# Performance work log

Measured on AMD Instinct MI355X. Metric: run time of the kernel, lower is better.

## Reference

```python
import jax, jax.numpy as jnp
import numpy as np
from jax import lax

DIM = 256
STATE = 64
D_INNER = 256          # ssd_expand=1 * dim
HIDDEN = 4 * DIM       # mlp_ratio=4
CONV_DIM = 3 * STATE
B, H, W = 16, 64, 64
EPS = 1e-5


def dwconv(x, w, b=None):
    # depthwise 3x3, SAME padding; x:(B,C,H,W) w:(C,1,3,3)
    y = lax.conv_general_dilated(x, w, (1, 1), 'SAME',
                                 feature_group_count=x.shape[1],
                                 dimension_numbers=('NCHW', 'OIHW', 'NCHW'))
    if b is not None:
        y = y + b[None, :, None, None]
    return y


def batchnorm(x, g, b):
    m = x.mean(axis=(0, 2, 3), keepdims=True)
    v = x.var(axis=(0, 2, 3), keepdims=True)
    return (x - m) * jax.lax.rsqrt(v + EPS) * g[None, :, None, None] + b[None, :, None, None]


def layernorm1d(x, w, b):
    # norm over channel dim of (B,C,L)
    m = x.mean(axis=1, keepdims=True)
    v = x.var(axis=1, keepdims=True)
    return (x - m) * jax.lax.rsqrt(v + EPS) * w[None, :, None] + b[None, :, None]


def pw1d(x, w, b):
    # 1x1 conv1d: x:(B,Cin,L), w:(Cout,Cin)
    return jnp.einsum('oc,bcl->bol', w, x) + b[None, :, None]


def setup_inputs() -> dict:
    key = jax.random.key(0)
    ks = jax.random.split(key, 16)
    s = 0.02
    inp = {
        'x': jax.random.normal(ks[0], (B, DIM, H, W), jnp.float32),
        'alpha': 1e-4 * jnp.ones((4, DIM), jnp.float32),
        'dw1_w': s * jax.random.normal(ks[1], (DIM, 1, 3, 3), jnp.float32),
        'bn1_g': jnp.ones((DIM,), jnp.float32),
        'bn1_b': jnp.zeros((DIM,), jnp.float32),
        'dw2_w': s * jax.random.normal(ks[2], (DIM, 1, 3, 3), jnp.float32),
        'bn2_g': jnp.ones((DIM,), jnp.float32),
        'bn2_b': jnp.zeros((DIM,), jnp.float32),
        'ln_w': jnp.ones((DIM,), jnp.float32),
        'ln_b': jnp.zeros((DIM,), jnp.float32),
        'bcdt_w': s * jax.random.normal(ks[3], (CONV_DIM, DIM), jnp.float32),
        'bcdt_b': jnp.zeros((CONV_DIM,), jnp.float32),
        'mdw_w': s * jax.random.normal(ks[4], (CONV_DIM, 1, 3, 3), jnp.float32),
        'mdw_b': jnp.zeros((CONV_DIM,), jnp.float32),
        'hz_w': s * jax.random.normal(ks[5], (2 * D_INNER, DIM), jnp.float32),
        'hz_b': jnp.zeros((2 * D_INNER,), jnp.float32),
        'out_w': s * jax.random.normal(ks[6], (DIM, D_INNER), jnp.float32),
        'out_b': jnp.zeros((DIM,), jnp.float32),
        'A': jax.random.uniform(ks[7], (STATE,), jnp.float32, 1.0, 16.0),
        'D': jnp.ones((1,), jnp.float32),
        'ffn_w1': s * jax.random.normal(ks[8], (HIDDEN, DIM), jnp.float32),
        'ffn_b1': jnp.zeros((HIDDEN,), jnp.float32),
        'ffn_w2': s * jax.random.normal(ks[9], (DIM, HIDDEN), jnp.float32),
        'ffn_b2': jnp.zeros((DIM,), jnp.float32),
    }
    return inp


def _mixer(xf, bcdt_w, bcdt_b, mdw_w, mdw_b, hz_w, hz_b, out_w, out_b, A, D, h_, w_):
    # xf: (B, dim, L)
    b = xf.shape[0]
    BCdt = pw1d(xf, bcdt_w, bcdt_b).reshape(b, CONV_DIM, h_, w_)
    BCdt = dwconv(BCdt, mdw_w, mdw_b).reshape(b, CONV_DIM, h_ * w_)
    Bm, Cm, dt = jnp.split(BCdt, [STATE, 2 * STATE], axis=1)  # (B,S,L) each
    Am = jax.nn.softmax(dt + A[None, :, None], axis=-1)
    AB = Am * Bm                                   # (B,S,L)
    h = jnp.einsum('bcl,bsl->bcs', xf, AB)         # (B,dim,S) small
    hz = jnp.einsum('oc,bcs->bos', hz_w, h) + hz_b[None, :, None]
    hh, z = jnp.split(hz, [D_INNER], axis=1)
    hh = hh * jax.nn.silu(z) + hh * D[0]
    hh = jnp.einsum('oc,bcs->bos', out_w, hh) + out_b[None, :, None]
    y = jnp.einsum('bcs,bsl->bcl', hh, Cm)         # (B,dim,L)
    return y.reshape(b, DIM, h_, w_)


def reference(x, alpha, dw1_w, bn1_g, bn1_b, dw2_w, bn2_g, bn2_b, ln_w, ln_b,
              bcdt_w, bcdt_b, mdw_w, mdw_b, hz_w, hz_b, out_w, out_b, A, D,
              ffn_w1, ffn_b1, ffn_w2, ffn_b2):
    a = jax.nn.sigmoid(alpha)[:, None, :, None, None]  # (4,1,dim,1,1)
    x = (1 - a[0]) * x + a[0] * batchnorm(dwconv(x, dw1_w), bn1_g, bn1_b)
    x_prev = x
    b, _, h_, w_ = x.shape
    xf = layernorm1d(x.reshape(b, DIM, h_ * w_), ln_w, ln_b)
    y = _mixer(xf, bcdt_w, bcdt_b, mdw_w, mdw_b, hz_w, hz_b, out_w, out_b, A, D, h_, w_)
    x = (1 - a[1]) * x_prev + a[1] * y
    x = (1 - a[2]) * x + a[2] * batchnorm(dwconv(x, dw2_w), bn2_g, bn2_b)
    # FFN: 1x1 conv -> GELU -> 1x1 conv
    hdn = jax.nn.gelu(jnp.einsum('oc,bchw->bohw', ffn_w1, x) + ffn_b1[None, :, None, None])
    x_ffn = jnp.einsum('oc,bchw->bohw', ffn_w2, hdn) + ffn_b2[None, :, None, None]
    x = (1 - a[3]) * x + a[3] * x_ffn
    return x
```

## Files before the change

### kernel.cpp

```cpp
#include <hip/hip_runtime.h>
#include <stdint.h>


typedef __attribute__((ext_vector_type(8))) short bf16x8;
typedef __attribute__((ext_vector_type(4))) float f32x4;

__device__ __forceinline__ unsigned short f2b(float f){
  union { float f; unsigned int u; } v; v.f = f;
  unsigned int r = v.u + 0x7FFFu + ((v.u >> 16) & 1u);
  return (unsigned short)(r >> 16);
}
__device__ __forceinline__ float b2f(unsigned short h){
  union { unsigned int u; float f; } v; v.u = ((unsigned int)h) << 16;
  return v.f;
}
__device__ __forceinline__ float sigm(float x){ return 1.0f / (1.0f + __expf(-x)); }
__device__ __forceinline__ float gelu_fast(float v){
  float t = v * (-2.3022059f - 0.10294886f * v * v);
  float e = __builtin_amdgcn_exp2f(t);
  return v * __builtin_amdgcn_rcpf(1.0f + e);
}
__device__ __forceinline__ unsigned int cvtpk(float lo, float hi){
  unsigned int r;
  asm volatile("v_cvt_pk_bf16_f32 %0, %1, %2" : "=v"(r) : "v"(lo), "v"(hi));
  return r;
}
__device__ __forceinline__ f32x4 mfma16(bf16x8 a, bf16x8 b, f32x4 c){
  return __builtin_amdgcn_mfma_f32_16x16x32_bf16(a, b, c, 0, 0, 0);
}
__device__ __forceinline__ bf16x8 ldb8g(const unsigned short* p){
  return *reinterpret_cast<const bf16x8*>(p);
}
__device__ __forceinline__ f32x4 zero4(){ f32x4 v = {0.f, 0.f, 0.f, 0.f}; return v; }
__device__ __forceinline__ void gload_lds16(const unsigned short* g, unsigned short* l){
  __builtin_amdgcn_global_load_lds(
      (const __attribute__((address_space(1))) void*)g,
      (__attribute__((address_space(3))) void*)l, 16, 0, 0);
}

__global__ __launch_bounds__(256) void k_setup(
    const float* __restrict__ w1, const float* __restrict__ w2,
    const float* __restrict__ bw, const float* __restrict__ hzw,
    const float* __restrict__ outw,
    unsigned short* __restrict__ w1b, unsigned short* __restrict__ w2b,
    unsigned short* __restrict__ bwb, unsigned short* __restrict__ hzwb,
    unsigned short* __restrict__ outwb){
  int tid = blockIdx.x * 256 + threadIdx.x;
  if (tid < 1024 * 256){ w1b[tid] = f2b(w1[tid]); w2b[tid] = f2b(w2[tid]); }
  if (tid < 192 * 256)  bwb[tid] = f2b(bw[tid]);
  if (tid < 512 * 256)  hzwb[tid] = f2b(hzw[tid]);
  if (tid < 256 * 256)  outwb[tid] = f2b(outw[tid]);
}

__global__ __launch_bounds__(256) void k_conv_stats(
    const float* __restrict__ x, const float* __restrict__ w,
    float* __restrict__ bnsum, float* __restrict__ bnsq){
  __shared__ float t[66 * 66];
  __shared__ float rs[4], rq[4];
  int bc = blockIdx.x; int c = bc & 255;
  const float* xp = x + (size_t)bc * 4096;
  int tid = threadIdx.x;
  for (int i = tid; i < 66 * 66; i += 256) t[i] = 0.f;
  __syncthreads();
  #pragma unroll
  for (int j = 0; j < 4; j++){
    int p4 = tid + j * 256;
    float4 v = reinterpret_cast<const float4*>(xp)[p4];
    int p = p4 * 4; int y = p >> 6, xx = p & 63;
    int base = (y + 1) * 66 + xx + 1;
    t[base] = v.x; t[base + 1] = v.y; t[base + 2] = v.z; t[base + 3] = v.w;
  }
  __syncthreads();
  float w0 = w[c*9+0], w1 = w[c*9+1], w2 = w[c*9+2], w3 = w[c*9+3], w4 = w[c*9+4];
  float w5 = w[c*9+5], w6 = w[c*9+6], w7 = w[c*9+7], w8 = w[c*9+8];
  float s = 0.f, q = 0.f;
  #pragma unroll
  for (int j = 0; j < 16; j++){
    int p = tid + j * 256; int y = p >> 6, xx = p & 63;
    const float* r0 = &t[y * 66 + xx];
    float v = r0[0]*w0 + r0[1]*w1 + r0[2]*w2 + r0[66]*w3 + r0[67]*w4 + r0[68]*w5
            + r0[132]*w6 + r0[133]*w7 + r0[134]*w8;
    s += v; q += v * v;
  }
  #pragma unroll
  for (int off = 32; off > 0; off >>= 1){ s += __shfl_down(s, off); q += __shfl_down(q, off); }
  if ((tid & 63) == 0){ rs[tid >> 6] = s; rq[tid >> 6] = q; }
  __syncthreads();
  if (tid == 0){
    atomicAdd(&bnsum[c], rs[0] + rs[1] + rs[2] + rs[3]);
    atomicAdd(&bnsq[c],  rq[0] + rq[1] + rq[2] + rq[3]);
  }
}

__global__ __launch_bounds__(256) void k_conv_bn_blend(
    const float* __restrict__ x, const float* __restrict__ w,
    const float* __restrict__ bnsum, const float* __restrict__ bnsq,
    const float* __restrict__ g, const float* __restrict__ bb,
    const float* __restrict__ alpha, float* __restrict__ out){
  __shared__ float t[66 * 66];
  int bc = blockIdx.x; int c = bc & 255;
  const float* xp = x + (size_t)bc * 4096;
  float* op = out + (size_t)bc * 4096;
  int tid = threadIdx.x;
  for (int i = tid; i < 66 * 66; i += 256) t[i] = 0.f;
  __syncthreads();
  #pragma unroll
  for (int j = 0; j < 4; j++){
    int p4 = tid + j * 256;
    float4 v = reinterpret_cast<const float4*>(xp)[p4];
    int p = p4 * 4; int y = p >> 6, xx = p & 63;
    int base = (y + 1) * 66 + xx + 1;
    t[base] = v.x; t[base + 1] = v.y; t[base + 2] = v.z; t[base + 3] = v.w;
  }
  __syncthreads();
  float w0 = w[c*9+0], w1 = w[c*9+1], w2 = w[c*9+2], w3 = w[c*9+3], w4 = w[c*9+4];
  float w5 = w[c*9+5], w6 = w[c*9+6], w7 = w[c*9+7], w8 = w[c*9+8];
  float m  = bnsum[c] * (1.f / 65536.f);
  float var = bnsq[c] * (1.f / 65536.f) - m * m;
  float sc = rsqrtf(var + 1e-5f) * g[c];
  float bias = bb[c];
  float a = sigm(alpha[c]);
  #pragma unroll
  for (int j = 0; j < 16; j++){
    int p = tid + j * 256; int y = p >> 6, xx = p & 63;
    const float* r0 = &t[y * 66 + xx];
    float v = r0[0]*w0 + r0[1]*w1 + r0[2]*w2 + r0[66]*w3 + r0[67]*w4 + r0[68]*w5
            + r0[132]*w6 + r0[133]*w7 + r0[134]*w8;
    float xv = t[(y + 1) * 66 + xx + 1];
    op[p] = (1.f - a) * xv + a * ((v - m) * sc + bias);
  }
}

__global__ __launch_bounds__(256) void k_ln(
    const float* __restrict__ x1, const float* __restrict__ lnw,
    const float* __restrict__ lnb, unsigned short* __restrict__ xf,
    unsigned short* __restrict__ xfT){
  __shared__ unsigned short st[256 * 65];
  __shared__ float reds[4][64], redq[4][64];
  int b = blockIdx.x >> 6, lt = blockIdx.x & 63; int l0 = lt * 64;
  int t = threadIdx.x, w = t >> 6, lane = t & 63;
  const float* xp = x1 + ((size_t)b * 256) * 4096 + l0 + lane;
  float s = 0.f, q = 0.f;
  for (int i = 0; i < 64; i++){
    int c = w * 64 + i;
    float v = xp[(size_t)c * 4096];
    s += v; q += v * v;
    st[c * 65 + lane] = f2b(v);
  }
  reds[w][lane] = s; redq[w][lane] = q;
  __syncthreads();
  s = reds[0][lane] + reds[1][lane] + reds[2][lane] + reds[3][lane];
  q = redq[0][lane] + redq[1][lane] + redq[2][lane] + redq[3][lane];
  float m = s * (1.f / 256.f);
  float r = rsqrtf(q * (1.f / 256.f) - m * m + 1e-5f);
  for (int i = 0; i < 64; i++){
    int c = w * 64 + i;
    float v = b2f(st[c * 65 + lane]);
    unsigned short h = f2b((v - m) * r * lnw[c] + lnb[c]);
    st[c * 65 + lane] = h;
    xf[((size_t)(b * 256 + c)) * 4096 + l0 + lane] = h;
  }
  __syncthreads();
  int p = t >> 4, cc = t & 15;
  for (int pi = 0; pi < 4; pi++){
    int px = p + pi * 16;
    #pragma unroll
    for (int j = 0; j < 2; j++){
      int c0 = (j * 16 + cc) * 8;
      unsigned short vv[8];
      #pragma unroll
      for (int k = 0; k < 8; k++) vv[k] = st[(c0 + k) * 65 + px];
      *reinterpret_cast<uint4*>(&xfT[((size_t)(b * 4096 + l0 + px)) * 256 + c0]) =
          *reinterpret_cast<uint4*>(vv);
    }
  }
}

__global__ __launch_bounds__(256) void k_xt(
    const float* __restrict__ x, unsigned short* __restrict__ xT){
  __shared__ unsigned short st[256 * 65];
  int b = blockIdx.x >> 6, lt = blockIdx.x & 63; int l0 = lt * 64;
  int t = threadIdx.x, w = t >> 6, lane = t & 63;
  const float* xp = x + ((size_t)b * 256) * 4096 + l0 + lane;
  for (int i = 0; i < 64; i++){
    int c = w * 64 + i;
    st[c * 65 + lane] = f2b(xp[(size_t)c * 4096]);
  }
  __syncthreads();
  int p = t >> 4, cc = t & 15;
  for (int pi = 0; pi < 4; pi++){
    int px = p + pi * 16;
    #pragma unroll
    for (int j = 0; j < 2; j++){
      int c0 = (j * 16 + cc) * 8;
      unsigned short vv[8];
      #pragma unroll
      for (int k = 0; k < 8; k++) vv[k] = st[(c0 + k) * 65 + px];
      *reinterpret_cast<uint4*>(&xT[((size_t)(b * 4096 + l0 + px)) * 256 + c0]) =
          *reinterpret_cast<uint4*>(vv);
    }
  }
}

__global__ __launch_bounds__(256) void k_bcdt(
    const unsigned short* __restrict__ xfT, const unsigned short* __restrict__ wb,
    const float* __restrict__ bias, unsigned short* __restrict__ outp){
  int blk = blockIdx.x; int b = blk >> 6, lt = blk & 63; int l0 = lt * 64;
  int t = threadIdx.x; int wv = t >> 6, lane = t & 63;
  int col = lane & 15, g = lane >> 4;
  f32x4 acc[3][4];
  #pragma unroll
  for (int mm = 0; mm < 3; mm++)
    #pragma unroll
    for (int nn = 0; nn < 4; nn++) acc[mm][nn] = zero4();
  for (int k = 0; k < 8; k++){
    bf16x8 av[3], bv[4];
    #pragma unroll
    for (int mm = 0; mm < 3; mm++){
      int o = (wv * 3 + mm) * 16 + col;
      av[mm] = ldb8g(&wb[(size_t)o * 256 + k * 32 + g * 8]);
    }
    #pragma unroll
    for (int nn = 0; nn < 4; nn++){
      int l = l0 + nn * 16 + col;
      bv[nn] = ldb8g(&xfT[((size_t)(b * 4096 + l)) * 256 + k * 32 + g * 8]);
    }
    #pragma unroll
    for (int mm = 0; mm < 3; mm++)
      #pragma unroll
      for (int nn = 0; nn < 4; nn++) acc[mm][nn] = mfma16(av[mm], bv[nn], acc[mm][nn]);
  }
  #pragma unroll
  for (int mm = 0; mm < 3; mm++)
    #pragma unroll
    for (int nn = 0; nn < 4; nn++)
      #pragma unroll
      for (int r = 0; r < 4; r++){
        int o = (wv * 3 + mm) * 16 + g * 4 + r;
        int l = l0 + nn * 16 + col;
        outp[((size_t)(b * 192 + o)) * 4096 + l] = f2b(acc[mm][nn][r] + bias[o]);
      }
}

__global__ __launch_bounds__(256) void k_conv_mid(
    const unsigned short* __restrict__ in, const float* __restrict__ w,
    const float* __restrict__ wbias, unsigned short* __restrict__ outp,
    float* __restrict__ smmax, float* __restrict__ smsum){
  __shared__ float t[66 * 66];
  __shared__ float red[8];
  int blk = blockIdx.x; int b = blk / 192, ch = blk % 192;
  const unsigned short* xp = in + (size_t)blk * 4096;
  unsigned short* op = outp + (size_t)blk * 4096;
  int tid = threadIdx.x;
  for (int i = tid; i < 66 * 66; i += 256) t[i] = 0.f;
  __syncthreads();
  #pragma unroll
  for (int j = 0; j < 2; j++){
    int p8 = tid + j * 256;
    unsigned short vv[8];
    *reinterpret_cast<uint4*>(vv) = reinterpret_cast<const uint4*>(xp)[p8];
    int p = p8 * 8; int y = p >> 6, xx = p & 63;
    int base = (y + 1) * 66 + xx + 1;
    #pragma unroll
    for (int k = 0; k < 8; k++) t[base + k] = b2f(vv[k]);
  }
  __syncthreads();
  float w0 = w[ch*9+0], w1 = w[ch*9+1], w2 = w[ch*9+2], w3 = w[ch*9+3], w4 = w[ch*9+4];
  float w5 = w[ch*9+5], w6 = w[ch*9+6], w7 = w[ch*9+7], w8 = w[ch*9+8];
  float bv = wbias[ch];
  float vloc[16];
  float mx = -1e30f;
  #pragma unroll
  for (int j = 0; j < 16; j++){
    int p = tid + j * 256; int y = p >> 6, xx = p & 63;
    const float* r0 = &t[y * 66 + xx];
    float v = r0[0]*w0 + r0[1]*w1 + r0[2]*w2 + r0[66]*w3 + r0[67]*w4 + r0[68]*w5
            + r0[132]*w6 + r0[133]*w7 + r0[134]*w8 + bv;
    unsigned short h = f2b(v);
    op[p] = h;
    float vb = b2f(h);
    vloc[j] = vb;
    mx = fmaxf(mx, vb);
  }
  if (ch >= 128){
    #pragma unroll
    for (int off = 32; off > 0; off >>= 1) mx = fmaxf(mx, __shfl_down(mx, off));
    if ((tid & 63) == 0) red[tid >> 6] = mx;
    __syncthreads();
    float M = fmaxf(fmaxf(red[0], red[1]), fmaxf(red[2], red[3]));
    float se = 0.f;
    #pragma unroll
    for (int j = 0; j < 16; j++) se += __expf(vloc[j] - M);
    #pragma unroll
    for (int off = 32; off > 0; off >>= 1) se += __shfl_down(se, off);
    if ((tid & 63) == 0) red[4 + (tid >> 6)] = se;
    __syncthreads();
    if (tid == 0){
      smmax[b * 64 + ch - 128] = M;
      smsum[b * 64 + ch - 128] = red[4] + red[5] + red[6] + red[7];
    }
  }
}

__global__ __launch_bounds__(256) void k_ab_cmt(
    const unsigned short* __restrict__ bc, const float* __restrict__ smmax,
    const float* __restrict__ smsum, unsigned short* __restrict__ ab,
    unsigned short* __restrict__ cmt){
  __shared__ float t[64 * 65];
  int blk = blockIdx.x;
  if (blk < 1024){
    int b = blk >> 6, s = blk & 63;
    const unsigned short* dt = bc + ((size_t)(b * 192 + 128 + s)) * 4096;
    const unsigned short* bm = bc + ((size_t)(b * 192 + s)) * 4096;
    unsigned short* o = ab + ((size_t)(b * 64 + s)) * 4096;
    float M = smmax[b * 64 + s];
    float inv = 1.f / smsum[b * 64 + s];
    for (int i = threadIdx.x; i < 4096; i += 256)
      o[i] = f2b(__expf(b2f(dt[i]) - M) * inv * b2f(bm[i]));
    return;
  }
  blk -= 1024;
  int b = blk >> 6, lt = blk & 63; int l0 = lt * 64;
  int tid = threadIdx.x;
  #pragma unroll
  for (int it = 0; it < 2; it++){
    int row = (tid >> 3) + it * 32;
    int lq = (tid & 7) * 8;
    const unsigned short* p = bc + ((size_t)(b * 192 + 64 + row)) * 4096 + l0 + lq;
    unsigned short vv[8];
    *reinterpret_cast<uint4*>(vv) = *reinterpret_cast<const uint4*>(p);
    #pragma unroll
    for (int k = 0; k < 8; k++) t[row * 65 + lq + k] = b2f(vv[k]);
  }
  __syncthreads();
  #pragma unroll
  for (int it = 0; it < 2; it++){
    int l = (tid >> 3) + it * 32;
    int sq = (tid & 7) * 8;
    unsigned short vv[8];
    #pragma unroll
    for (int k = 0; k < 8; k++) vv[k] = f2b(t[(sq + k) * 65 + l]);
    *reinterpret_cast<uint4*>(&cmt[((size_t)(b * 4096 + l0 + l)) * 64 + sq]) =
        *reinterpret_cast<uint4*>(vv);
  }
}

__global__ __launch_bounds__(512) void k_h(
    const unsigned short* __restrict__ ab, const unsigned short* __restrict__ xf,
    float* __restrict__ hpart){
  int blk = blockIdx.x; int b = blk & 15, chunk = blk >> 4;
  int t = threadIdx.x; int wv = t >> 6, lane = t & 63;
  int col = lane & 15, g = lane >> 4;
  int mt = wv & 3, nh = wv >> 2;
  f32x4 acc[8];
  #pragma unroll
  for (int nn = 0; nn < 8; nn++) acc[nn] = zero4();
  int lbase = chunk * 256;
  const unsigned short* ap = ab + ((size_t)(b * 64 + mt * 16 + col)) * 4096 + lbase + g * 8;
  for (int ks = 0; ks < 8; ks++){
    bf16x8 av = ldb8g(ap + ks * 32);
    #pragma unroll
    for (int nn = 0; nn < 8; nn++){
      int c = nh * 128 + nn * 16 + col;
      bf16x8 bv = ldb8g(&xf[((size_t)(b * 256 + c)) * 4096 + lbase + ks * 32 + g * 8]);
      acc[nn] = mfma16(av, bv, acc[nn]);
    }
  }
  #pragma unroll
  for (int nn = 0; nn < 8; nn++)
    #pragma unroll
    for (int r = 0; r < 4; r++){
      int s = mt * 16 + g * 4 + r;
      int c = nh * 128 + nn * 16 + col;
      hpart[(((size_t)chunk * 16 + b) * 64 + s) * 256 + c] = acc[nn][r];
    }
}

__global__ __launch_bounds__(256) void k_hsum(
    const float* __restrict__ hp, unsigned short* __restrict__ hsb){
  int i = blockIdx.x * 256 + threadIdx.x;
  float s = 0.f;
  #pragma unroll
  for (int c = 0; c < 16; c++) s += hp[(size_t)c * 262144 + i];
  hsb[i] = f2b(s);
}

__global__ __launch_bounds__(256) void k_hz(
    const unsigned short* __restrict__ hsb, const unsigned short* __restrict__ hzwb,
    const float* __restrict__ hzb, const float* __restrict__ Dp,
    unsigned short* __restrict__ hh1b){
  int blk = blockIdx.x; int b = blk >> 2, og = blk & 3;
  int t = threadIdx.x, wv = t >> 6, lane = t & 63;
  int col = lane & 15, g = lane >> 4;
  int ou = og * 64 + wv * 16;
  int oz = 256 + ou;
  f32x4 au[4], az[4];
  #pragma unroll
  for (int nn = 0; nn < 4; nn++){ au[nn] = zero4(); az[nn] = zero4(); }
  const unsigned short* bbase = hsb + (size_t)b * 64 * 256;
  for (int k = 0; k < 8; k++){
    bf16x8 a_u = ldb8g(&hzwb[(size_t)(ou + col) * 256 + k * 32 + g * 8]);
    bf16x8 a_z = ldb8g(&hzwb[(size_t)(oz + col) * 256 + k * 32 + g * 8]);
    bf16x8 bv[4];
    #pragma unroll
    for (int nn = 0; nn < 4; nn++)
      bv[nn] = ldb8g(bbase + (size_t)(nn * 16 + col) * 256 + k * 32 + g * 8);
    #pragma unroll
    for (int nn = 0; nn < 4; nn++){
      au[nn] = mfma16(a_u, bv[nn], au[nn]);
      az[nn] = mfma16(a_z, bv[nn], az[nn]);
    }
  }
  float Dv = Dp[0];
  #pragma unroll
  for (int nn = 0; nn < 4; nn++){
    int s = nn * 16 + col;
    float hv[4];
    #pragma unroll
    for (int r = 0; r < 4; r++){
      int o = ou + g * 4 + r;
      float u = au[nn][r] + hzb[o];
      float z = az[nn][r] + hzb[o + 256];
      float sl = z / (1.f + __expf(-z));
      hv[r] = u * (sl + Dv);
    }
    unsigned int p0 = cvtpk(hv[0], hv[1]), p1 = cvtpk(hv[2], hv[3]);
    uint2 pv; pv.x = p0; pv.y = p1;
    *reinterpret_cast<uint2*>(&hh1b[((size_t)(b * 64 + s)) * 256 + ou + g * 4]) = pv;
  }
}

__global__ __launch_bounds__(256) void k_out(
    const unsigned short* __restrict__ hh1b, const unsigned short* __restrict__ outwb,
    const float* __restrict__ ob, unsigned short* __restrict__ hh2){
  int blk = blockIdx.x; int b = blk >> 2, dg = blk & 3;
  int t = threadIdx.x, wv = t >> 6, lane = t & 63;
  int col = lane & 15, g = lane >> 4;
  int d0 = dg * 64 + wv * 16;
  f32x4 acc[4];
  #pragma unroll
  for (int nn = 0; nn < 4; nn++) acc[nn] = zero4();
  const unsigned short* bbase = hh1b + (size_t)b * 64 * 256;
  for (int k = 0; k < 8; k++){
    bf16x8 a = ldb8g(&outwb[(size_t)(d0 + col) * 256 + k * 32 + g * 8]);
    bf16x8 bv[4];
    #pragma unroll
    for (int nn = 0; nn < 4; nn++)
      bv[nn] = ldb8g(bbase + (size_t)(nn * 16 + col) * 256 + k * 32 + g * 8);
    #pragma unroll
    for (int nn = 0; nn < 4; nn++) acc[nn] = mfma16(a, bv[nn], acc[nn]);
  }
  #pragma unroll
  for (int nn = 0; nn < 4; nn++){
    int s = nn * 16 + col;
    #pragma unroll
    for (int r = 0; r < 4; r++){
      int d = d0 + g * 4 + r;
      hh2[((size_t)(b * 256 + d)) * 64 + s] = f2b(acc[nn][r] + ob[d]);
    }
  }
}

__global__ __launch_bounds__(256) void k_y_blend(
    const unsigned short* __restrict__ hh2, const unsigned short* __restrict__ cmt,
    const float* __restrict__ alpha, float* __restrict__ x){
  int blk = blockIdx.x; int b = blk >> 6, lt = blk & 63; int l0 = lt * 64;
  int t = threadIdx.x; int wv = t >> 6, lane = t & 63;
  int col = lane & 15, g = lane >> 4;
  f32x4 acc[4][4];
  #pragma unroll
  for (int mm = 0; mm < 4; mm++)
    #pragma unroll
    for (int nn = 0; nn < 4; nn++) acc[mm][nn] = zero4();
  #pragma unroll
  for (int k = 0; k < 2; k++){
    bf16x8 av[4], bv[4];
    #pragma unroll
    for (int mm = 0; mm < 4; mm++){
      int c = (wv * 4 + mm) * 16 + col;
      av[mm] = ldb8g(&hh2[((size_t)(b * 256 + c)) * 64 + k * 32 + g * 8]);
    }
    #pragma unroll
    for (int nn = 0; nn < 4; nn++){
      int l = l0 + nn * 16 + col;
      bv[nn] = ldb8g(&cmt[((size_t)(b * 4096 + l)) * 64 + k * 32 + g * 8]);
    }
    #pragma unroll
    for (int mm = 0; mm < 4; mm++)
      #pragma unroll
      for (int nn = 0; nn < 4; nn++) acc[mm][nn] = mfma16(av[mm], bv[nn], acc[mm][nn]);
  }
  #pragma unroll
  for (int mm = 0; mm < 4; mm++)
    #pragma unroll
    for (int r = 0; r < 4; r++){
      int c = (wv * 4 + mm) * 16 + g * 4 + r;
      float a1 = sigm(alpha[c]);
      #pragma unroll
      for (int nn = 0; nn < 4; nn++){
        int l = l0 + nn * 16 + col;
        size_t idx = ((size_t)(b * 256 + c)) * 4096 + l;
        float xv = x[idx];
        x[idx] = (1.f - a1) * xv + a1 * acc[mm][nn][r];
      }
    }
}

__global__ __launch_bounds__(256, 4) void k_ffn1(
    const unsigned short* __restrict__ xT, const unsigned short* __restrict__ w1b,
    const float* __restrict__ b1, unsigned short* __restrict__ Hh, int b0){
  __shared__ unsigned short smem[17408];
  unsigned short* At = smem;
  unsigned short* Bt = smem + 8192;
  int wk = ((blockIdx.x & 7) << 8) + (blockIdx.x >> 3);
  int mt = wk & 7, nt = wk >> 3;
  int t = threadIdx.x, wv = t >> 6, lane = t & 63;
  int col = lane & 15, g = lane >> 4;
  int wr = wv >> 1, wc = wv & 1;
  const unsigned short* ag = w1b + (size_t)(mt * 128) * 256;
  const unsigned short* bg = xT + ((size_t)b0 * 4096 + (size_t)nt * 128) * 256;
  float bias[4][4];
  #pragma unroll
  for (int mm = 0; mm < 4; mm++)
    #pragma unroll
    for (int r = 0; r < 4; r++)
      bias[mm][r] = b1[mt * 128 + wr * 64 + mm * 16 + g * 4 + r];
  f32x4 acc[4][4];
  #pragma unroll
  for (int mm = 0; mm < 4; mm++)
    #pragma unroll
    for (int nn = 0; nn < 4; nn++) acc[mm][nn] = zero4();
  for (int kk = 0; kk < 4; kk++){
    __syncthreads();
    #pragma unroll
    for (int j = 0; j < 4; j++){
      int id = t + j * 256;
      int row = id >> 3, kc = (id & 7) * 8;
      gload_lds16(ag + (size_t)row * 256 + kk * 64 + kc, At + id * 8);
      gload_lds16(bg + (size_t)row * 256 + kk * 64 + kc, Bt + id * 8);
    }
    __syncthreads();
    #pragma unroll
    for (int ks = 0; ks < 2; ks++){
      bf16x8 av[4], bv[4];
      #pragma unroll
      for (int mm = 0; mm < 4; mm++)
        av[mm] = *reinterpret_cast<const bf16x8*>(&At[(wr * 64 + mm * 16 + col) * 64 + ks * 32 + g * 8]);
      #pragma unroll
      for (int nn = 0; nn < 4; nn++)
        bv[nn] = *reinterpret_cast<const bf16x8*>(&Bt[(wc * 64 + nn * 16 + col) * 64 + ks * 32 + g * 8]);
      #pragma unroll
      for (int mm = 0; mm < 4; mm++)
        #pragma unroll
        for (int nn = 0; nn < 4; nn++)
          acc[mm][nn] = mfma16(av[mm], bv[nn], acc[mm][nn]);
    }
  }
  __syncthreads();
  #pragma unroll
  for (int mm = 0; mm < 4; mm++){
    int o4 = wr * 64 + mm * 16 + g * 4;
    #pragma unroll
    for (int nn = 0; nn < 4; nn++){
      int lloc = wc * 64 + nn * 16 + col;
      float gv[4];
      #pragma unroll
      for (int r = 0; r < 4; r++)
        gv[r] = gelu_fast(acc[mm][nn][r] + bias[mm][r]);
      uint2 pv; pv.x = cvtpk(gv[0], gv[1]); pv.y = cvtpk(gv[2], gv[3]);
      *reinterpret_cast<uint2*>(&smem[lloc * 136 + o4]) = pv;
    }
  }
  __syncthreads();
  size_t hb = (size_t)nt * 128;
  #pragma unroll
  for (int j = 0; j < 8; j++){
    int id = t + j * 256;
    int l = id >> 4, oc = id & 15;
    uint4 v = *reinterpret_cast<const uint4*>(&smem[l * 136 + oc * 8]);
    *reinterpret_cast<uint4*>(&Hh[(hb + l) * 1024 + mt * 128 + oc * 8]) = v;
  }
}

__global__ __launch_bounds__(256, 4) void k_ffn2(
    const unsigned short* __restrict__ Hh, const unsigned short* __restrict__ w2b,
    const float* __restrict__ b2, const float* __restrict__ alpha3,
    float* __restrict__ x, int b0){
  __shared__ unsigned short At[128 * 64];
  __shared__ unsigned short Bt[64 * 64];
  int wk = ((blockIdx.x & 7) << 7) + (blockIdx.x >> 3);
  int mt = wk & 1, nt = wk >> 1;
  int t = threadIdx.x, wv = t >> 6, lane = t & 63;
  int col = lane & 15, g = lane >> 4;
  int wr = wv >> 1, wc = wv & 1;
  const unsigned short* ag = w2b + (size_t)(mt * 128) * 1024;
  const unsigned short* bg = Hh + (size_t)(nt * 64) * 1024;
  f32x4 acc[4][2];
  #pragma unroll
  for (int mm = 0; mm < 4; mm++)
    #pragma unroll
    for (int nn = 0; nn < 2; nn++) acc[mm][nn] = zero4();
  for (int kk = 0; kk < 16; kk++){
    __syncthreads();
    #pragma unroll
    for (int j = 0; j < 4; j++){
      int id = t + j * 256;
      int row = id >> 3, kc = (id & 7) * 8;
      gload_lds16(ag + (size_t)row * 1024 + kk * 64 + kc, At + id * 8);
    }
    #pragma unroll
    for (int j = 0; j < 2; j++){
      int id = t + j * 256;
      int row = id >> 3, kc = (id & 7) * 8;
      gload_lds16(bg + (size_t)row * 1024 + kk * 64 + kc, Bt + id * 8);
    }
    __syncthreads();
    #pragma unroll
    for (int ks = 0; ks < 2; ks++){
      bf16x8 av[4], bv[2];
      #pragma unroll
      for (int mm = 0; mm < 4; mm++)
        av[mm] = *reinterpret_cast<const bf16x8*>(&At[(wr * 64 + mm * 16 + col) * 64 + ks * 32 + g * 8]);
      #pragma unroll
      for (int nn = 0; nn < 2; nn++)
        bv[nn] = *reinterpret_cast<const bf16x8*>(&Bt[(wc * 32 + nn * 16 + col) * 64 + ks * 32 + g * 8]);
      #pragma unroll
      for (int mm = 0; mm < 4; mm++)
        #pragma unroll
        for (int nn = 0; nn < 2; nn++)
          acc[mm][nn] = mfma16(av[mm], bv[nn], acc[mm][nn]);
    }
  }
  #pragma unroll
  for (int mm = 0; mm < 4; mm++)
    #pragma unroll
    for (int r = 0; r < 4; r++){
      int d = mt * 128 + wr * 64 + mm * 16 + g * 4 + r;
      float a3 = sigm(alpha3[d]);
      float bias = b2[d];
      #pragma unroll
      for (int nn = 0; nn < 2; nn++){
        int lh = nt * 64 + wc * 32 + nn * 16 + col;
        int b = b0 + (lh >> 12);
        int l = lh & 4095;
        size_t idx = ((size_t)(b * 256 + d)) * 4096 + l;
        float xv = x[idx];
        x[idx] = (1.f - a3) * xv + a3 * (acc[mm][nn][r] + bias);
      }
    }
}

extern "C" void kernel_launch(void* const* d_in, const int* in_sizes, int n_in,
                              void* d_out, int out_size, void* d_ws, size_t ws_size,
                              hipStream_t stream){
  (void)in_sizes; (void)n_in; (void)out_size; (void)ws_size;
  const float* x      = (const float*)d_in[0];
  const float* alpha  = (const float*)d_in[1];
  const float* dw1_w  = (const float*)d_in[2];
  const float* bn1_g  = (const float*)d_in[3];
  const float* bn1_b  = (const float*)d_in[4];
  const float* dw2_w  = (const float*)d_in[5];
  const float* bn2_g  = (const float*)d_in[6];
  const float* bn2_b  = (const float*)d_in[7];
  const float* ln_w   = (const float*)d_in[8];
  const float* ln_b   = (const float*)d_in[9];
  const float* bcdt_w = (const float*)d_in[10];
  const float* bcdt_b = (const float*)d_in[11];
  const float* mdw_w  = (const float*)d_in[12];
  const float* mdw_b  = (const float*)d_in[13];
  const float* hz_w   = (const float*)d_in[14];
  const float* hz_b   = (const float*)d_in[15];
  const float* out_w  = (const float*)d_in[16];
  const float* out_b  = (const float*)d_in[17];
  const float* Dvec   = (const float*)d_in[19];
  const float* ffn_w1 = (const float*)d_in[20];
  const float* ffn_b1 = (const float*)d_in[21];
  const float* ffn_w2 = (const float*)d_in[22];
  const float* ffn_b2 = (const float*)d_in[23];
  float* out = (float*)d_out;
  char* ws = (char*)d_ws;

  const size_t OFF_BCRAW = 0;
  const size_t OFF_BCC   = 25165824;
  const size_t OFF_XF    = 50331648;
  const size_t OFF_XFT   = 83886080;
  const size_t OFF_AB    = 0;
  const size_t OFF_CMT   = 8388608;
  const size_t OFF_HPART = 16777216;
  const size_t OFF_HSB   = 83886080;
  const size_t OFF_HH1B  = 84410368;
  const size_t OFF_HH2   = 84934656;
  const size_t OFF_H     = 0;
  const size_t OFF_X3T   = 67108864;
  const size_t OFF_W1B   = 117440512;
  const size_t OFF_W2B   = 117964800;
  const size_t OFF_BWB   = 118489088;
  const size_t OFF_HZWB  = 118587392;
  const size_t OFF_OUTWB = 119111680;
  const size_t OFF_STATS = 119373824;
  const size_t OFF_SMMAX = 119377920;
  const size_t OFF_SMSUM = 119382016;

  unsigned short* bcraw = (unsigned short*)(ws + OFF_BCRAW);
  unsigned short* bcc   = (unsigned short*)(ws + OFF_BCC);
  unsigned short* xf    = (unsigned short*)(ws + OFF_XF);
  unsigned short* xfT   = (unsigned short*)(ws + OFF_XFT);
  unsigned short* ab    = (unsigned short*)(ws + OFF_AB);
  unsigned short* cmt   = (unsigned short*)(ws + OFF_CMT);
  float* hpart = (float*)(ws + OFF_HPART);
  unsigned short* hsb  = (unsigned short*)(ws + OFF_HSB);
  unsigned short* hh1b = (unsigned short*)(ws + OFF_HH1B);
  unsigned short* hh2  = (unsigned short*)(ws + OFF_HH2);
  unsigned short* Hbuf = (unsigned short*)(ws + OFF_H);
  unsigned short* x3T  = (unsigned short*)(ws + OFF_X3T);
  unsigned short* w1b = (unsigned short*)(ws + OFF_W1B);
  unsigned short* w2b = (unsigned short*)(ws + OFF_W2B);
  unsigned short* bwb = (unsigned short*)(ws + OFF_BWB);
  unsigned short* hzwb  = (unsigned short*)(ws + OFF_HZWB);
  unsigned short* outwb = (unsigned short*)(ws + OFF_OUTWB);
  float* bn1sum = (float*)(ws + OFF_STATS);
  float* bn1sq  = bn1sum + 256;
  float* bn2sum = bn1sum + 512;
  float* bn2sq  = bn1sum + 768;
  float* smmax = (float*)(ws + OFF_SMMAX);
  float* smsum = (float*)(ws + OFF_SMSUM);

  hipMemsetAsync(ws + OFF_STATS, 0, 4096, stream);
  k_setup<<<1024, 256, 0, stream>>>(ffn_w1, ffn_w2, bcdt_w, hz_w, out_w,
                                    w1b, w2b, bwb, hzwb, outwb);
  k_conv_stats<<<4096, 256, 0, stream>>>(x, dw1_w, bn1sum, bn1sq);
  k_conv_bn_blend<<<4096, 256, 0, stream>>>(x, dw1_w, bn1sum, bn1sq,
                                            bn1_g, bn1_b, alpha + 0, out);
  k_ln<<<1024, 256, 0, stream>>>(out, ln_w, ln_b, xf, xfT);
  k_bcdt<<<1024, 256, 0, stream>>>(xfT, bwb, bcdt_b, bcraw);
  k_conv_mid<<<3072, 256, 0, stream>>>(bcraw, mdw_w, mdw_b, bcc, smmax, smsum);
  k_ab_cmt<<<2048, 256, 0, stream>>>(bcc, smmax, smsum, ab, cmt);
  k_h<<<256, 512, 0, stream>>>(ab, xf, hpart);
  k_hsum<<<1024, 256, 0, stream>>>(hpart, hsb);
  k_hz<<<64, 256, 0, stream>>>(hsb, hzwb, hz_b, Dvec, hh1b);
  k_out<<<64, 256, 0, stream>>>(hh1b, outwb, out_b, hh2);
  k_y_blend<<<1024, 256, 0, stream>>>(hh2, cmt, alpha + 256, out);
  k_conv_stats<<<4096, 256, 0, stream>>>(out, dw2_w, bn2sum, bn2sq);
  k_conv_bn_blend<<<4096, 256, 0, stream>>>(out, dw2_w, bn2sum, bn2sq,
                                            bn2_g, bn2_b, alpha + 512, out);
  k_xt<<<1024, 256, 0, stream>>>(out, x3T);
  k_ffn1<<<2048, 256, 0, stream>>>(x3T, w1b, ffn_b1, Hbuf, 0);
  k_ffn2<<<1024, 256, 0, stream>>>(Hbuf, w2b, ffn_b2, alpha + 768, out, 0);
  k_ffn1<<<2048, 256, 0, stream>>>(x3T, w1b, ffn_b1, Hbuf, 8);
  k_ffn2<<<1024, 256, 0, stream>>>(Hbuf, w2b, ffn_b2, alpha + 768, out, 8);
}
```

Measured before the change: 387.3 us.

## Store intermediate residual stream in bf16 instead of fp32

The residual activation passed between stages (after the first conv/BN blend, the mixer blend, the second conv/BN blend, and the FFN residual read) is now kept in a bf16 workspace buffer instead of fp32 in the output buffer. New kernel variants read and write bf16 for the conv stats, conv-BN blend, LN, transpose and y-blend steps, and ffn2 reads the bf16 residual and writes fp32 output. The workspace layout is reorganised to make room. This roughly halves the memory traffic of these bandwidth-bound passes, at the cost of extra rounding error on the residual path.

```diff
diff --git a/kernel.cpp b/kernel.cpp
--- a/kernel.cpp
+++ b/kernel.cpp
@@ -92,15 +92,57 @@
   }
 }
 
-__global__ __launch_bounds__(256) void k_conv_bn_blend(
+__global__ __launch_bounds__(256) void k_conv_stats_h(
+    const unsigned short* __restrict__ x, const float* __restrict__ w,
+    float* __restrict__ bnsum, float* __restrict__ bnsq){
+  __shared__ float t[66 * 66];
+  __shared__ float rs[4], rq[4];
+  int bc = blockIdx.x; int c = bc & 255;
+  const unsigned short* xp = x + (size_t)bc * 4096;
+  int tid = threadIdx.x;
+  for (int i = tid; i < 66 * 66; i += 256) t[i] = 0.f;
+  __syncthreads();
+  #pragma unroll
+  for (int j = 0; j < 2; j++){
+    int p8 = tid + j * 256;
+    unsigned short vv[8];
+    *reinterpret_cast<uint4*>(vv) = reinterpret_cast<const uint4*>(xp)[p8];
+    int p = p8 * 8; int y = p >> 6, xx = p & 63;
+    int base = (y + 1) * 66 + xx + 1;
+    #pragma unroll
+    for (int k = 0; k < 8; k++) t[base + k] = b2f(vv[k]);
+  }
+  __syncthreads();
+  float w0 = w[c*9+0], w1 = w[c*9+1], w2 = w[c*9+2], w3 = w[c*9+3], w4 = w[c*9+4];
+  float w5 = w[c*9+5], w6 = w[c*9+6], w7 = w[c*9+7], w8 = w[c*9+8];
+  float s = 0.f, q = 0.f;
+  #pragma unroll
+  for (int j = 0; j < 16; j++){
+    int p = tid + j * 256; int y = p >> 6, xx = p & 63;
+    const float* r0 = &t[y * 66 + xx];
+    float v = r0[0]*w0 + r0[1]*w1 + r0[2]*w2 + r0[66]*w3 + r0[67]*w4 + r0[68]*w5
+            + r0[132]*w6 + r0[133]*w7 + r0[134]*w8;
+    s += v; q += v * v;
+  }
+  #pragma unroll
+  for (int off = 32; off > 0; off >>= 1){ s += __shfl_down(s, off); q += __shfl_down(q, off); }
+  if ((tid & 63) == 0){ rs[tid >> 6] = s; rq[tid >> 6] = q; }
+  __syncthreads();
+  if (tid == 0){
+    atomicAdd(&bnsum[c], rs[0] + rs[1] + rs[2] + rs[3]);
+    atomicAdd(&bnsq[c],  rq[0] + rq[1] + rq[2] + rq[3]);
+  }
+}
+
+__global__ __launch_bounds__(256) void k_conv_bn_blend_f2h(
     const float* __restrict__ x, const float* __restrict__ w,
     const float* __restrict__ bnsum, const float* __restrict__ bnsq,
     const float* __restrict__ g, const float* __restrict__ bb,
-    const float* __restrict__ alpha, float* __restrict__ out){
+    const float* __restrict__ alpha, unsigned short* __restrict__ out){
   __shared__ float t[66 * 66];
   int bc = blockIdx.x; int c = bc & 255;
   const float* xp = x + (size_t)bc * 4096;
-  float* op = out + (size_t)bc * 4096;
+  unsigned short* op = out + (size_t)bc * 4096;
   int tid = threadIdx.x;
   for (int i = tid; i < 66 * 66; i += 256) t[i] = 0.f;
   __syncthreads();
@@ -127,25 +169,67 @@
     float v = r0[0]*w0 + r0[1]*w1 + r0[2]*w2 + r0[66]*w3 + r0[67]*w4 + r0[68]*w5
             + r0[132]*w6 + r0[133]*w7 + r0[134]*w8;
     float xv = t[(y + 1) * 66 + xx + 1];
-    op[p] = (1.f - a) * xv + a * ((v - m) * sc + bias);
+    op[p] = f2b((1.f - a) * xv + a * ((v - m) * sc + bias));
+  }
+}
+
+__global__ __launch_bounds__(256) void k_conv_bn_blend_h2h(
+    const unsigned short* __restrict__ x, const float* __restrict__ w,
+    const float* __restrict__ bnsum, const float* __restrict__ bnsq,
+    const float* __restrict__ g, const float* __restrict__ bb,
+    const float* __restrict__ alpha, unsigned short* __restrict__ out){
+  __shared__ float t[66 * 66];
+  int bc = blockIdx.x; int c = bc & 255;
+  const unsigned short* xp = x + (size_t)bc * 4096;
+  unsigned short* op = out + (size_t)bc * 4096;
+  int tid = threadIdx.x;
+  for (int i = tid; i < 66 * 66; i += 256) t[i] = 0.f;
+  __syncthreads();
+  #pragma unroll
+  for (int j = 0; j < 2; j++){
+    int p8 = tid + j * 256;
+    unsigned short vv[8];
+    *reinterpret_cast<uint4*>(vv) = reinterpret_cast<const uint4*>(xp)[p8];
+    int p = p8 * 8; int y = p >> 6, xx = p & 63;
+    int base = (y + 1) * 66 + xx + 1;
+    #pragma unroll
+    for (int k = 0; k < 8; k++) t[base + k] = b2f(vv[k]);
+  }
+  __syncthreads();
+  float w0 = w[c*9+0], w1 = w[c*9+1], w2 = w[c*9+2], w3 = w[c*9+3], w4 = w[c*9+4];
+  float w5 = w[c*9+5], w6 = w[c*9+6], w7 = w[c*9+7], w8 = w[c*9+8];
+  float m  = bnsum[c] * (1.f / 65536.f);
+  float var = bnsq[c] * (1.f / 65536.f) - m * m;
+  float sc = rsqrtf(var + 1e-5f) * g[c];
+  float bias = bb[c];
+  float a = sigm(alpha[c]);
+  #pragma unroll
+  for (int j = 0; j < 16; j++){
+    int p = tid + j * 256; int y = p >> 6, xx = p & 63;
+    const float* r0 = &t[y * 66 + xx];
+    float v = r0[0]*w0 + r0[1]*w1 + r0[2]*w2 + r0[66]*w3 + r0[67]*w4 + r0[68]*w5
+            + r0[132]*w6 + r0[133]*w7 + r0[134]*w8;
+    float xv = t[(y + 1) * 66 + xx + 1];
+    op[p] = f2b((1.f - a) * xv + a * ((v - m) * sc + bias));
   }
 }
 
 __global__ __launch_bounds__(256) void k_ln(
-    const float* __restrict__ x1, const float* __restrict__ lnw,
+    const unsigned short* __restrict__ x1, const float* __restrict__ lnw,
     const float* __restrict__ lnb, unsigned short* __restrict__ xf,
     unsigned short* __restrict__ xfT){
   __shared__ unsigned short st[256 * 65];
   __shared__ float reds[4][64], redq[4][64];
   int b = blockIdx.x >> 6, lt = blockIdx.x & 63; int l0 = lt * 64;
   int t = threadIdx.x, w = t >> 6, lane = t & 63;
-  const float* xp = x1 + ((size_t)b * 256) * 4096 + l0 + lane;
+  const unsigned short* xp = x1 + ((size_t)b * 256) * 4096 + l0 + lane;
   float s = 0.f, q = 0.f;
   for (int i = 0; i < 64; i++){
     int c = w * 64 + i;
-    float v = xp[(size_t)c * 4096];
+    unsigned short h = xp[(size_t)c * 4096];
+    float v = b2f(h);
     s += v; q += v * v;
-    st[c * 65 + lane] = f2b(v);
+    st[c * 65 + lane] = h;
   }
   reds[w][lane] = s; redq[w][lane] = q;
   __syncthreads();
@@ -177,14 +261,14 @@
 }
 
 __global__ __launch_bounds__(256) void k_xt(
-    const float* __restrict__ x, unsigned short* __restrict__ xT){
+    const unsigned short* __restrict__ x, unsigned short* __restrict__ xT){
   __shared__ unsigned short st[256 * 65];
   int b = blockIdx.x >> 6, lt = blockIdx.x & 63; int l0 = lt * 64;
   int t = threadIdx.x, w = t >> 6, lane = t & 63;
-  const float* xp = x + ((size_t)b * 256) * 4096 + l0 + lane;
+  const unsigned short* xp = x + ((size_t)b * 256) * 4096 + l0 + lane;
   for (int i = 0; i < 64; i++){
     int c = w * 64 + i;
-    st[c * 65 + lane] = f2b(xp[(size_t)c * 4096]);
+    st[c * 65 + lane] = xp[(size_t)c * 4096];
   }
   __syncthreads();
   int p = t >> 4, cc = t & 15;
@@ -463,7 +547,7 @@
 
 __global__ __launch_bounds__(256) void k_y_blend(
     const unsigned short* __restrict__ hh2, const unsigned short* __restrict__ cmt,
-    const float* __restrict__ alpha, float* __restrict__ x){
+    const float* __restrict__ alpha, unsigned short* __restrict__ x){
   int blk = blockIdx.x; int b = blk >> 6, lt = blk & 63; int l0 = lt * 64;
   int t = threadIdx.x; int wv = t >> 6, lane = t & 63;
   int col = lane & 15, g = lane >> 4;
@@ -500,8 +584,8 @@
       for (int nn = 0; nn < 4; nn++){
         int l = l0 + nn * 16 + col;
         size_t idx = ((size_t)(b * 256 + c)) * 4096 + l;
-        float xv = x[idx];
-        x[idx] = (1.f - a1) * xv + a1 * acc[mm][nn][r];
+        float xv = b2f(x[idx]);
+        x[idx] = f2b((1.f - a1) * xv + a1 * acc[mm][nn][r]);
       }
     }
 }
@@ -585,7 +669,7 @@
 __global__ __launch_bounds__(256, 4) void k_ffn2(
     const unsigned short* __restrict__ Hh, const unsigned short* __restrict__ w2b,
     const float* __restrict__ b2, const float* __restrict__ alpha3,
-    float* __restrict__ x, int b0){
+    const unsigned short* __restrict__ xres, float* __restrict__ outp, int b0){
   __shared__ unsigned short At[128 * 64];
   __shared__ unsigned short Bt[64 * 64];
   int wk = ((blockIdx.x & 7) << 7) + (blockIdx.x >> 3);
@@ -644,8 +728,8 @@
         int b = b0 + (lh >> 12);
         int l = lh & 4095;
         size_t idx = ((size_t)(b * 256 + d)) * 4096 + l;
-        float xv = x[idx];
-        x[idx] = (1.f - a3) * xv + a3 * (acc[mm][nn][r] + bias);
+        float xv = b2f(xres[idx]);
+        outp[idx] = (1.f - a3) * xv + a3 * (acc[mm][nn][r] + bias);
       }
     }
 }
@@ -680,44 +764,46 @@
   float* out = (float*)d_out;
   char* ws = (char*)d_ws;
 
-  const size_t OFF_BCRAW = 0;
-  const size_t OFF_BCC   = 25165824;
-  const size_t OFF_XF    = 50331648;
-  const size_t OFF_XFT   = 83886080;
-  const size_t OFF_AB    = 0;
-  const size_t OFF_CMT   = 8388608;
-  const size_t OFF_HPART = 16777216;
-  const size_t OFF_HSB   = 83886080;
-  const size_t OFF_HH1B  = 84410368;
-  const size_t OFF_HH2   = 84934656;
-  const size_t OFF_H     = 0;
-  const size_t OFF_X3T   = 67108864;
-  const size_t OFF_W1B   = 117440512;
-  const size_t OFF_W2B   = 117964800;
-  const size_t OFF_BWB   = 118489088;
-  const size_t OFF_HZWB  = 118587392;
-  const size_t OFF_OUTWB = 119111680;
-  const size_t OFF_STATS = 119373824;
-  const size_t OFF_SMMAX = 119377920;
-  const size_t OFF_SMSUM = 119382016;
-
-  unsigned short* bcraw = (unsigned short*)(ws + OFF_BCRAW);
-  unsigned short* bcc   = (unsigned short*)(ws + OFF_BCC);
+  const size_t OFF_XRES  = 0;
+  const size_t OFF_XF    = 33554432;
+  const size_t OFF_XFT   = 67108864;
+  const size_t OFF_BCC   = 67108864;
+  const size_t OFF_BCRAW = 100663296;
+  const size_t OFF_AB    = 100663296;
+  const size_t OFF_CMT   = 109051904;
+  const size_t OFF_HPART = 117440512;
+  const size_t OFF_X3T   = 33554432;
+  const size_t OFF_H     = 67108864;
+  const size_t OFF_W1B   = 134217728;
+  const size_t OFF_W2B   = 134742016;
+  const size_t OFF_BWB   = 135266304;
+  const size_t OFF_HZWB  = 135364608;
+  const size_t OFF_OUTWB = 135626752;
+  const size_t OFF_HSB   = 135757824;
+  const size_t OFF_HH1B  = 136282112;
+  const size_t OFF_HH2   = 136806400;
+  const size_t OFF_STATS = 137330688;
+  const size_t OFF_SMMAX = 137334784;
+  const size_t OFF_SMSUM = 137338880;
+
+  unsigned short* xres  = (unsigned short*)(ws + OFF_XRES);
   unsigned short* xf    = (unsigned short*)(ws + OFF_XF);
   unsigned short* xfT   = (unsigned short*)(ws + OFF_XFT);
+  unsigned short* bcc   = (unsigned short*)(ws + OFF_BCC);
+  unsigned short* bcraw = (unsigned short*)(ws + OFF_BCRAW);
   unsigned short* ab    = (unsigned short*)(ws + OFF_AB);
   unsigned short* cmt   = (unsigned short*)(ws + OFF_CMT);
   float* hpart = (float*)(ws + OFF_HPART);
-  unsigned short* hsb  = (unsigned short*)(ws + OFF_HSB);
-  unsigned short* hh1b = (unsigned short*)(ws + OFF_HH1B);
-  unsigned short* hh2  = (unsigned short*)(ws + OFF_HH2);
+  unsigned short* x3T  = (unsigned short*)(ws + OFF_X3T);
   unsigned short* Hbuf = (unsigned short*)(ws + OFF_H);
-  unsigned short* x3T  = (unsigned short*)(ws + OFF_X3T);
   unsigned short* w1b = (unsigned short*)(ws + OFF_W1B);
   unsigned short* w2b = (unsigned short*)(ws + OFF_W2B);
   unsigned short* bwb = (unsigned short*)(ws + OFF_BWB);
   unsigned short* hzwb  = (unsigned short*)(ws + OFF_HZWB);
   unsigned short* outwb = (unsigned short*)(ws + OFF_OUTWB);
+  unsigned short* hsb  = (unsigned short*)(ws + OFF_HSB);
+  unsigned short* hh1b = (unsigned short*)(ws + OFF_HH1B);
+  unsigned short* hh2  = (unsigned short*)(ws + OFF_HH2);
   float* bn1sum = (float*)(ws + OFF_STATS);
   float* bn1sq  = bn1sum + 256;
   float* bn2sum = bn1sum + 512;
@@ -729,9 +815,9 @@
   k_setup<<<1024, 256, 0, stream>>>(ffn_w1, ffn_w2, bcdt_w, hz_w, out_w,
                                     w1b, w2b, bwb, hzwb, outwb);
   k_conv_stats<<<4096, 256, 0, stream>>>(x, dw1_w, bn1sum, bn1sq);
-  k_conv_bn_blend<<<4096, 256, 0, stream>>>(x, dw1_w, bn1sum, bn1sq,
-                                            bn1_g, bn1_b, alpha + 0, out);
-  k_ln<<<1024, 256, 0, stream>>>(out, ln_w, ln_b, xf, xfT);
+  k_conv_bn_blend_f2h<<<4096, 256, 0, stream>>>(x, dw1_w, bn1sum, bn1sq,
+                                                bn1_g, bn1_b, alpha + 0, xres);
+  k_ln<<<1024, 256, 0, stream>>>(xres, ln_w, ln_b, xf, xfT);
   k_bcdt<<<1024, 256, 0, stream>>>(xfT, bwb, bcdt_b, bcraw);
   k_conv_mid<<<3072, 256, 0, stream>>>(bcraw, mdw_w, mdw_b, bcc, smmax, smsum);
   k_ab_cmt<<<2048, 256, 0, stream>>>(bcc, smmax, smsum, ab, cmt);
@@ -739,13 +825,13 @@
   k_hsum<<<1024, 256, 0, stream>>>(hpart, hsb);
   k_hz<<<64, 256, 0, stream>>>(hsb, hzwb, hz_b, Dvec, hh1b);
   k_out<<<64, 256, 0, stream>>>(hh1b, outwb, out_b, hh2);
-  k_y_blend<<<1024, 256, 0, stream>>>(hh2, cmt, alpha + 256, out);
-  k_conv_stats<<<4096, 256, 0, stream>>>(out, dw2_w, bn2sum, bn2sq);
-  k_conv_bn_blend<<<4096, 256, 0, stream>>>(out, dw2_w, bn2sum, bn2sq,
-                                            bn2_g, bn2_b, alpha + 512, out);
-  k_xt<<<1024, 256, 0, stream>>>(out, x3T);
+  k_y_blend<<<1024, 256, 0, stream>>>(hh2, cmt, alpha + 256, xres);
+  k_conv_stats_h<<<4096, 256, 0, stream>>>(xres, dw2_w, bn2sum, bn2sq);
+  k_conv_bn_blend_h2h<<<4096, 256, 0, stream>>>(xres, dw2_w, bn2sum, bn2sq,
+                                                bn2_g, bn2_b, alpha + 512, xres);
+  k_xt<<<1024, 256, 0, stream>>>(xres, x3T);
   k_ffn1<<<2048, 256, 0, stream>>>(x3T, w1b, ffn_b1, Hbuf, 0);
-  k_ffn2<<<1024, 256, 0, stream>>>(Hbuf, w2b, ffn_b2, alpha + 768, out, 0);
+  k_ffn2<<<1024, 256, 0, stream>>>(Hbuf, w2b, ffn_b2, alpha + 768, xres, out, 0);
   k_ffn1<<<2048, 256, 0, stream>>>(x3T, w1b, ffn_b1, Hbuf, 8);
-  k_ffn2<<<1024, 256, 0, stream>>>(Hbuf, w2b, ffn_b2, alpha + 768, out, 8);
-}
+  k_ffn2<<<1024, 256, 0, stream>>>(Hbuf, w2b, ffn_b2, alpha + 768, xres, out, 8);
+}
```

Measured after the change: 358.9 us (median of 2 runs). -7.3%, faster.
